# Kernel tuning notes

Measured on AMD Instinct MI355X. Metric: run time of the kernel, lower is better.

The kernel has to match this reference:

```python
import jax, jax.numpy as jnp
import numpy as np
from jax import lax

B, C, H, W = 8, 256, 64, 64
O, K, E = 256, 3, 3  # out_channels, kernel_size, num_experts

def setup_inputs() -> dict:
    key = jax.random.key(0)
    k1, k2, k3, k4, k5 = jax.random.split(key, 5)
    q = jax.random.normal(k1, (B, C, H, W), dtype=jnp.float32)
    y = jax.random.normal(k2, (B, C, H, W), dtype=jnp.float32)
    experts = jax.random.normal(k3, (E, O, 2 * C, K, K), dtype=jnp.float32)
    # torch nn.Linear(2C, E): store transposed [2C, E] for ctx @ gate_w
    bound = 1.0 / np.sqrt(2 * C)
    gate_w = jax.random.uniform(k4, (2 * C, E), minval=-bound, maxval=bound, dtype=jnp.float32)
    gate_b = jax.random.uniform(k5, (E,), minval=-bound, maxval=bound, dtype=jnp.float32)
    return {"q": q, "y": y, "experts": experts, "gate_w": gate_w, "gate_b": gate_b}

def reference(q, y, experts, gate_w, gate_b):
    # gate: softmax over experts from global-avg-pooled context of y (duplicated)
    y_ctx = jnp.mean(y, axis=(2, 3))                       # [B, C]
    context = jnp.concatenate([y_ctx, y_ctx], axis=1)       # [B, 2C]
    gates = jax.nn.softmax(context @ gate_w + gate_b, axis=1)  # [B, E]
    # per-sample fused kernel: sum_e gates[b,e] * experts[e]  -> [B, O, 2C, K, K]
    w = jnp.einsum('be,eoikl->boikl', gates, experts)
    xy = jnp.concatenate([q, q], axis=1)                     # [B, 2C, H, W]
    # batched dynamic conv via grouped conv: batch -> groups (no Python loop)
    b, c2, h, wd = xy.shape
    x1 = xy.reshape(1, b * c2, h, wd)
    w1 = w.reshape(b * O, c2, K, K)
    out = lax.conv_general_dilated(
        x1, w1, window_strides=(1, 1), padding='SAME',
        dimension_numbers=('NCHW', 'OIHW', 'NCHW'),
        feature_group_count=b)
    return out.reshape(b, O, h, wd)
```

## Files before the change

kernel.cpp:

```cpp
#include <hip/hip_runtime.h>
#include <hip/hip_bf16.h>
#include <math.h>


typedef __bf16 bf16x8 __attribute__((ext_vector_type(8)));
typedef __bf16 bf16x4 __attribute__((ext_vector_type(4)));
typedef float f32x4 __attribute__((ext_vector_type(4)));

#define AS1 __attribute__((address_space(1)))
#define AS3 __attribute__((address_space(3)))

__global__ __launch_bounds__(64) void yctx_kernel(const float* __restrict__ y,
                                                  float* __restrict__ yctx) {
  int bc = blockIdx.x;
  const float4* p = (const float4*)(y + (size_t)bc * 4096);
  int lane = threadIdx.x;
  float s = 0.f;
  for (int i = lane; i < 1024; i += 64) {
    float4 v = p[i];
    s += v.x + v.y + v.z + v.w;
  }
#pragma unroll
  for (int off = 32; off > 0; off >>= 1) s += __shfl_down(s, off, 64);
  if (lane == 0) yctx[bc] = s * (1.f / 4096.f);
}

__global__ __launch_bounds__(64) void logits_kernel(const float* __restrict__ yctx,
                                                    const float* __restrict__ gw,
                                                    const float* __restrict__ gb,
                                                    float* __restrict__ logits) {
  int be = blockIdx.x;
  int b = be / 3, e = be - b * 3;
  int lane = threadIdx.x;
  float s = 0.f;
  for (int c = lane; c < 256; c += 64)
    s += yctx[b * 256 + c] * (gw[c * 3 + e] + gw[(c + 256) * 3 + e]);
#pragma unroll
  for (int off = 32; off > 0; off >>= 1) s += __shfl_down(s, off, 64);
  if (lane == 0) logits[be] = s + gb[e];
}

__global__ __launch_bounds__(256) void wbuild_kernel(const float* __restrict__ experts,
                                                     const float* __restrict__ logits,
                                                     __bf16* __restrict__ wf) {
  int o = blockIdx.x;
  int tid = threadIdx.x;
  __shared__ float sf[3][2304];
  __shared__ float g[8][3];

#pragma unroll
  for (int e = 0; e < 3; e++) {
    const float4* src = (const float4*)(experts + ((size_t)e * 256 + o) * 4608);
    float4* dstp = (float4*)sf[e];
    for (int i = tid; i < 576; i += 256) {
      float4 a = src[i], bq = src[i + 576];
      float4 r;
      r.x = a.x + bq.x; r.y = a.y + bq.y; r.z = a.z + bq.z; r.w = a.w + bq.w;
      dstp[i] = r;
    }
  }
  if (tid < 8) {
    float l0 = logits[tid * 3 + 0], l1 = logits[tid * 3 + 1], l2 = logits[tid * 3 + 2];
    float m = fmaxf(l0, fmaxf(l1, l2));
    float e0 = __expf(l0 - m), e1 = __expf(l1 - m), e2 = __expf(l2 - m);
    float inv = 1.f / (e0 + e1 + e2);
    g[tid][0] = e0 * inv; g[tid][1] = e1 * inv; g[tid][2] = e2 * inv;
  }
  __syncthreads();

  int cl = tid & 31, ch = tid >> 5;
#pragma unroll 1
  for (int b = 0; b < 8; b++) {
    float g0 = g[b][0], g1 = g[b][1], g2 = g[b][2];
#pragma unroll
    for (int tap = 0; tap < 9; tap++) {
      float v = g0 * sf[0][tid * 9 + tap] + g1 * sf[1][tid * 9 + tap] +
                g2 * sf[2][tid * 9 + tap];
      wf[((((size_t)b * 9 + tap) * 8 + ch) * 256 + o) * 32 + cl] = (__bf16)v;
    }
  }
}

__global__ __launch_bounds__(256) void qt_kernel(const float* __restrict__ q,
                                                 __bf16* __restrict__ qT) {
  int bid = blockIdx.x;
  int hp = bid % 66;
  int t2 = bid / 66;
  int ch = t2 & 7;
  int b = t2 >> 3;
  __bf16* dst = qT + (((size_t)(b * 8 + ch) * 66 + hp) * 66) * 32;
  int tid = threadIdx.x;
  float4 z4 = {0.f, 0.f, 0.f, 0.f};
  if (hp == 0 || hp == 65) {
    float4* d4 = (float4*)dst;
    for (int i = tid; i < 264; i += 256) d4[i] = z4;
    return;
  }
  __shared__ float tile2[64][33];
  int h = hp - 1;
  {
    int w = tid & 63, ci = tid >> 6;
#pragma unroll
    for (int j = 0; j < 8; j++) {
      int c = ci * 8 + j;
      tile2[w][c] = q[(((size_t)b * 256 + ch * 32 + c) * 64 + h) * 64 + w];
    }
  }
  if (tid < 4) ((float4*)dst)[tid] = z4;
  else if (tid < 8) ((float4*)(dst + 65 * 32))[tid - 4] = z4;
  __syncthreads();

  int a = tid & 7, wsl = tid >> 3;
  int cl4 = a * 4;
#pragma unroll
  for (int k = 0; k < 2; k++) {
    int w = wsl * 2 + k, wp = w + 1;
    int clp4 = (((cl4 >> 3) ^ ((wp >> 1) & 3)) << 3) | (cl4 & 7);
    float v0 = tile2[w][cl4 + 0], v1 = tile2[w][cl4 + 1];
    float v2 = tile2[w][cl4 + 2], v3 = tile2[w][cl4 + 3];
    bf16x4 r = {(__bf16)v0, (__bf16)v1, (__bf16)v2, (__bf16)v3};
    *(bf16x4*)(dst + wp * 32 + clp4) = r;
  }
}

__global__ __launch_bounds__(256, 2) void conv_kernel(const __bf16* __restrict__ qT,
                                                      const __bf16* __restrict__ wf,
                                                      float* __restrict__ out) {
  __shared__ __align__(16) __bf16 Qlds[2][4 * 66 * 32];
  const int tid = threadIdx.x;
  const int lane = tid & 63;
  const int wv = tid >> 6;
  const int wm = wv >> 1, wn = wv & 1;
  const int l15 = lane & 15, qd = lane >> 4;

  const int bid = blockIdx.x;
  const int b = bid & 7;
  const int rem = bid >> 3;
  const int o0 = (rem >> 5) * 128;
  const int h0 = (rem & 31) * 2;

  f32x4 acc[4][4];
  {
    f32x4 z = {0.f, 0.f, 0.f, 0.f};
#pragma unroll
    for (int i = 0; i < 4; i++)
#pragma unroll
      for (int j = 0; j < 4; j++) acc[i][j] = z;
  }

  int btab[3][4];
#pragma unroll
  for (int dw = 0; dw < 3; dw++)
#pragma unroll
    for (int ni = 0; ni < 4; ni++) {
      int wp = ni * 16 + l15 + dw;
      int g = (qd ^ ((wp >> 1) & 3)) << 3;
      btab[dw][ni] = (wp * 32 + g) * 2;
    }

  const char* qT_b = (const char*)qT + (size_t)b * 8 * 66 * 66 * 32 * 2;
  const char* abase = (const char*)wf + ((size_t)b * 9 * 8 * 256 +
                                         (size_t)(o0 + wm * 64 + l15)) * 64 +
                      (size_t)qd * 16;
  bf16x8 areg[3][4];
  bf16x8 breg[2][4];

  {
    const char* qsrc = qT_b + ((size_t)h0) * 4224;
    for (int i = tid; i < 1056; i += 256) {
      int ub = i - lane;
      __builtin_amdgcn_global_load_lds((const AS1 void*)(qsrc + ((size_t)i << 4)),
                                       (AS3 void*)((char*)Qlds[0] + ((size_t)ub << 4)),
                                       16, 0, 0);
    }
#pragma unroll
    for (int mi = 0; mi < 4; mi++) {
      areg[0][mi] = *(const bf16x8*)(abase + ((size_t)(0 * 8 + 0) << 14) + mi * 1024);
      areg[1][mi] = *(const bf16x8*)(abase + ((size_t)(1 * 8 + 0) << 14) + mi * 1024);
    }
    __syncthreads();
#pragma unroll
    for (int ni = 0; ni < 4; ni++)
      breg[0][ni] = *(const bf16x8*)((const char*)Qlds[0] + wn * 4224 + btab[0][ni]);
  }

#pragma unroll 1
  for (int ch = 0; ch < 8; ch++) {
    if (ch < 7) {
      const char* qsrc = qT_b + ((size_t)((ch + 1) * 66 + h0)) * 4224;
      char* qdst = (char*)Qlds[(ch + 1) & 1];
      for (int i = tid; i < 1056; i += 256) {
        int ub = i - lane;
        __builtin_amdgcn_global_load_lds((const AS1 void*)(qsrc + ((size_t)i << 4)),
                                         (AS3 void*)(qdst + ((size_t)ub << 4)),
                                         16, 0, 0);
      }
    }
    const char* Qb = (const char*)Qlds[ch & 1];
#pragma unroll
    for (int tap = 0; tap < 9; tap++) {
      const int s = ch * 9 + tap;
      {
        int s2 = s + 2;
        int ch2 = s2 / 9, tap2 = s2 - ch2 * 9;
        if (ch2 > 7) { ch2 = 0; tap2 = 0; }
        size_t aoff = ((size_t)(tap2 * 8 + ch2)) << 14;
#pragma unroll
        for (int mi = 0; mi < 4; mi++)
          areg[(s + 2) % 3][mi] = *(const bf16x8*)(abase + aoff + mi * 1024);
      }
      if (tap < 8) {
        int tapn = tap + 1;
        int dhn = tapn / 3, dwn = tapn - dhn * 3;
        int rbn = (wn + dhn) * 4224;
#pragma unroll
        for (int ni = 0; ni < 4; ni++)
          breg[(tap + 1) & 1][ni] = *(const bf16x8*)(Qb + rbn + btab[dwn][ni]);
      }
#pragma unroll
      for (int ni = 0; ni < 4; ni++)
#pragma unroll
        for (int mi = 0; mi < 4; mi++)
          acc[mi][ni] = __builtin_amdgcn_mfma_f32_16x16x32_bf16(
              areg[s % 3][mi], breg[tap & 1][ni], acc[mi][ni], 0, 0, 0);
    }
    __syncthreads();
    if (ch < 7) {
      const char* Qn = (const char*)Qlds[(ch + 1) & 1];
#pragma unroll
      for (int ni = 0; ni < 4; ni++)
        breg[0][ni] = *(const bf16x8*)(Qn + wn * 4224 + btab[0][ni]);
    }
  }

  const int hh = h0 + wn;
#pragma unroll
  for (int mi = 0; mi < 4; mi++) {
    int o = o0 + wm * 64 + mi * 16 + qd * 4;
#pragma unroll
    for (int ni = 0; ni < 4; ni++) {
      int w = ni * 16 + l15;
#pragma unroll
      for (int rr = 0; rr < 4; rr++)
        out[(((size_t)b * 256 + (o + rr)) * 64 + hh) * 64 + w] = acc[mi][ni][rr];
    }
  }
}

extern "C" void kernel_launch(void* const* d_in, const int* in_sizes, int n_in,
                              void* d_out, int out_size, void* d_ws, size_t ws_size,
                              hipStream_t stream) {
  (void)in_sizes; (void)n_in; (void)out_size; (void)ws_size;
  const float* q = (const float*)d_in[0];
  const float* y = (const float*)d_in[1];
  const float* experts = (const float*)d_in[2];
  const float* gate_w = (const float*)d_in[3];
  const float* gate_b = (const float*)d_in[4];
  float* out = (float*)d_out;

  char* ws = (char*)d_ws;
  float* yctx = (float*)ws;
  float* logits = (float*)(ws + 8192);
  __bf16* wf = (__bf16*)(ws + 16384);
  __bf16* qT = (__bf16*)(ws + 16384 + 9437184);

  yctx_kernel<<<2048, 64, 0, stream>>>(y, yctx);
  logits_kernel<<<24, 64, 0, stream>>>(yctx, gate_w, gate_b, logits);
  qt_kernel<<<8 * 8 * 66, 256, 0, stream>>>(q, qT);
  wbuild_kernel<<<256, 256, 0, stream>>>(experts, logits, wf);
  conv_kernel<<<512, 256, 0, stream>>>(qT, wf, out);
}
```

Baseline: 182.9 us.

## Fuse prep kernels and switch conv to 32x32x16 MFMA tiles

Merges the y-mean and q-transpose kernels into one launch, and folds the gate logits computation into the weight-build kernel, cutting five launches to three. The conv kernel switches from 16x16x32 to 32x32x16 bf16 MFMA with 2x2 tiles per wave and remaps the A and B fragment offsets to match. Fewer, larger MFMAs aim to cut LDS and register fragment traffic per FLOP. The output write pattern changes to the 32x32 accumulator layout, which may coalesce differently.

```diff
diff --git a/kernel.cpp b/kernel.cpp
--- a/kernel.cpp
+++ b/kernel.cpp
@@ -6,46 +6,78 @@
 typedef __bf16 bf16x8 __attribute__((ext_vector_type(8)));
 typedef __bf16 bf16x4 __attribute__((ext_vector_type(4)));
 typedef float f32x4 __attribute__((ext_vector_type(4)));
+typedef float f32x16 __attribute__((ext_vector_type(16)));
 
 #define AS1 __attribute__((address_space(1)))
 #define AS3 __attribute__((address_space(3)))
 
-__global__ __launch_bounds__(64) void yctx_kernel(const float* __restrict__ y,
-                                                  float* __restrict__ yctx) {
-  int bc = blockIdx.x;
-  const float4* p = (const float4*)(y + (size_t)bc * 4096);
-  int lane = threadIdx.x;
-  float s = 0.f;
-  for (int i = lane; i < 1024; i += 64) {
-    float4 v = p[i];
-    s += v.x + v.y + v.z + v.w;
-  }
-#pragma unroll
-  for (int off = 32; off > 0; off >>= 1) s += __shfl_down(s, off, 64);
-  if (lane == 0) yctx[bc] = s * (1.f / 4096.f);
+__global__ __launch_bounds__(256) void prep_kernel(const float* __restrict__ q,
+                                                   const float* __restrict__ y,
+                                                   __bf16* __restrict__ qT,
+                                                   float* __restrict__ yctx) {
+  int bid = blockIdx.x;
+  int tid = threadIdx.x;
+  if (bid >= 4224) {
+    int wv = tid >> 6, lane = tid & 63;
+    int bc = (bid - 4224) * 4 + wv;
+    const float4* p = (const float4*)(y + (size_t)bc * 4096);
+    float s = 0.f;
+    for (int i = lane; i < 1024; i += 64) {
+      float4 v = p[i];
+      s += v.x + v.y + v.z + v.w;
+    }
+#pragma unroll
+    for (int off = 32; off > 0; off >>= 1) s += __shfl_down(s, off, 64);
+    if (lane == 0) yctx[bc] = s * (1.f / 4096.f);
+    return;
+  }
+  int hp = bid % 66;
+  int t2 = bid / 66;
+  int ch = t2 & 7;
+  int b = t2 >> 3;
+  __bf16* dst = qT + (((size_t)(b * 8 + ch) * 66 + hp) * 66) * 32;
+  float4 z4 = {0.f, 0.f, 0.f, 0.f};
+  if (hp == 0 || hp == 65) {
+    float4* d4 = (float4*)dst;
+    for (int i = tid; i < 264; i += 256) d4[i] = z4;
+    return;
+  }
+  __shared__ float tile2[64][33];
+  int h = hp - 1;
+  {
+    int w = tid & 63, ci = tid >> 6;
+#pragma unroll
+    for (int j = 0; j < 8; j++) {
+      int c = ci * 8 + j;
+      tile2[w][c] = q[(((size_t)b * 256 + ch * 32 + c) * 64 + h) * 64 + w];
+    }
+  }
+  if (tid < 4) ((float4*)dst)[tid] = z4;
+  else if (tid < 8) ((float4*)(dst + 65 * 32))[tid - 4] = z4;
+  __syncthreads();
+
+  int a = tid & 7, wsl = tid >> 3;
+  int cl4 = a * 4;
+#pragma unroll
+  for (int k = 0; k < 2; k++) {
+    int w = wsl * 2 + k, wp = w + 1;
+    int clp4 = (((cl4 >> 3) ^ ((wp >> 1) & 3)) << 3) | (cl4 & 7);
+    float v0 = tile2[w][cl4 + 0], v1 = tile2[w][cl4 + 1];
+    float v2 = tile2[w][cl4 + 2], v3 = tile2[w][cl4 + 3];
+    bf16x4 r = {(__bf16)v0, (__bf16)v1, (__bf16)v2, (__bf16)v3};
+    *(bf16x4*)(dst + wp * 32 + clp4) = r;
+  }
 }
 
-__global__ __launch_bounds__(64) void logits_kernel(const float* __restrict__ yctx,
-                                                    const float* __restrict__ gw,
-                                                    const float* __restrict__ gb,
-                                                    float* __restrict__ logits) {
-  int be = blockIdx.x;
-  int b = be / 3, e = be - b * 3;
-  int lane = threadIdx.x;
-  float s = 0.f;
-  for (int c = lane; c < 256; c += 64)
-    s += yctx[b * 256 + c] * (gw[c * 3 + e] + gw[(c + 256) * 3 + e]);
-#pragma unroll
-  for (int off = 32; off > 0; off >>= 1) s += __shfl_down(s, off, 64);
-  if (lane == 0) logits[be] = s + gb[e];
-}
-
 __global__ __launch_bounds__(256) void wbuild_kernel(const float* __restrict__ experts,
-                                                     const float* __restrict__ logits,
+                                                     const float* __restrict__ yctx,
+                                                     const float* __restrict__ gw,
+                                                     const float* __restrict__ gb,
                                                      __bf16* __restrict__ wf) {
   int o = blockIdx.x;
   int tid = threadIdx.x;
   __shared__ float sf[3][2304];
+  __shared__ float lgpart[4][24];
   __shared__ float g[8][3];
 
 #pragma unroll
@@ -59,8 +91,34 @@
       dstp[i] = r;
     }
   }
+  {
+    int c = tid;
+    float gwf[3], yc[8];
+#pragma unroll
+    for (int e = 0; e < 3; e++) gwf[e] = gw[c * 3 + e] + gw[(c + 256) * 3 + e];
+#pragma unroll
+    for (int b = 0; b < 8; b++) yc[b] = yctx[b * 256 + c];
+    int wv = tid >> 6, lane = tid & 63;
+#pragma unroll
+    for (int b = 0; b < 8; b++)
+#pragma unroll
+      for (int e = 0; e < 3; e++) {
+        float s = yc[b] * gwf[e];
+#pragma unroll
+        for (int off = 32; off > 0; off >>= 1) s += __shfl_down(s, off, 64);
+        if (lane == 0) lgpart[wv][b * 3 + e] = s;
+      }
+  }
+  __syncthreads();
+  if (tid < 24) {
+    int e = tid % 3;
+    float s = lgpart[0][tid] + lgpart[1][tid] + lgpart[2][tid] + lgpart[3][tid] + gb[e];
+    lgpart[0][tid] = s;
+  }
+  __syncthreads();
   if (tid < 8) {
-    float l0 = logits[tid * 3 + 0], l1 = logits[tid * 3 + 1], l2 = logits[tid * 3 + 2];
+    float l0 = lgpart[0][tid * 3 + 0], l1 = lgpart[0][tid * 3 + 1],
+          l2 = lgpart[0][tid * 3 + 2];
     float m = fmaxf(l0, fmaxf(l1, l2));
     float e0 = __expf(l0 - m), e1 = __expf(l1 - m), e2 = __expf(l2 - m);
     float inv = 1.f / (e0 + e1 + e2);
@@ -78,48 +136,6 @@
                 g2 * sf[2][tid * 9 + tap];
       wf[((((size_t)b * 9 + tap) * 8 + ch) * 256 + o) * 32 + cl] = (__bf16)v;
     }
-  }
-}
-
-__global__ __launch_bounds__(256) void qt_kernel(const float* __restrict__ q,
-                                                 __bf16* __restrict__ qT) {
-  int bid = blockIdx.x;
-  int hp = bid % 66;
-  int t2 = bid / 66;
-  int ch = t2 & 7;
-  int b = t2 >> 3;
-  __bf16* dst = qT + (((size_t)(b * 8 + ch) * 66 + hp) * 66) * 32;
-  int tid = threadIdx.x;
-  float4 z4 = {0.f, 0.f, 0.f, 0.f};
-  if (hp == 0 || hp == 65) {
-    float4* d4 = (float4*)dst;
-    for (int i = tid; i < 264; i += 256) d4[i] = z4;
-    return;
-  }
-  __shared__ float tile2[64][33];
-  int h = hp - 1;
-  {
-    int w = tid & 63, ci = tid >> 6;
-#pragma unroll
-    for (int j = 0; j < 8; j++) {
-      int c = ci * 8 + j;
-      tile2[w][c] = q[(((size_t)b * 256 + ch * 32 + c) * 64 + h) * 64 + w];
-    }
-  }
-  if (tid < 4) ((float4*)dst)[tid] = z4;
-  else if (tid < 8) ((float4*)(dst + 65 * 32))[tid - 4] = z4;
-  __syncthreads();
-
-  int a = tid & 7, wsl = tid >> 3;
-  int cl4 = a * 4;
-#pragma unroll
-  for (int k = 0; k < 2; k++) {
-    int w = wsl * 2 + k, wp = w + 1;
-    int clp4 = (((cl4 >> 3) ^ ((wp >> 1) & 3)) << 3) | (cl4 & 7);
-    float v0 = tile2[w][cl4 + 0], v1 = tile2[w][cl4 + 1];
-    float v2 = tile2[w][cl4 + 2], v3 = tile2[w][cl4 + 3];
-    bf16x4 r = {(__bf16)v0, (__bf16)v1, (__bf16)v2, (__bf16)v3};
-    *(bf16x4*)(dst + wp * 32 + clp4) = r;
   }
 }
 
@@ -131,7 +147,7 @@
   const int lane = tid & 63;
   const int wv = tid >> 6;
   const int wm = wv >> 1, wn = wv & 1;
-  const int l15 = lane & 15, qd = lane >> 4;
+  const int l31 = lane & 31, hi = lane >> 5;
 
   const int bid = blockIdx.x;
   const int b = bid & 7;
@@ -139,29 +155,31 @@
   const int o0 = (rem >> 5) * 128;
   const int h0 = (rem & 31) * 2;
 
-  f32x4 acc[4][4];
+  f32x16 acc[2][2];
   {
-    f32x4 z = {0.f, 0.f, 0.f, 0.f};
-#pragma unroll
-    for (int i = 0; i < 4; i++)
-#pragma unroll
-      for (int j = 0; j < 4; j++) acc[i][j] = z;
-  }
-
-  int btab[3][4];
+    f32x16 z = {0.f};
+#pragma unroll
+    for (int i = 0; i < 2; i++)
+#pragma unroll
+      for (int j = 0; j < 2; j++) acc[i][j] = z;
+  }
+
+  int bofs[3][2][2];
 #pragma unroll
   for (int dw = 0; dw < 3; dw++)
 #pragma unroll
-    for (int ni = 0; ni < 4; ni++) {
-      int wp = ni * 16 + l15 + dw;
-      int g = (qd ^ ((wp >> 1) & 3)) << 3;
-      btab[dw][ni] = (wp * 32 + g) * 2;
+    for (int nt = 0; nt < 2; nt++) {
+      int wp = nt * 32 + l31 + dw;
+      int sw = (wp >> 1) & 3;
+#pragma unroll
+      for (int kh = 0; kh < 2; kh++)
+        bofs[dw][nt][kh] = wp * 64 + (((kh * 2 + hi) ^ sw) << 4);
     }
 
   const char* qT_b = (const char*)qT + (size_t)b * 8 * 66 * 66 * 32 * 2;
   const char* abase = (const char*)wf + ((size_t)b * 9 * 8 * 256 +
-                                         (size_t)(o0 + wm * 64 + l15)) * 64 +
-                      (size_t)qd * 16;
+                                         (size_t)(o0 + wm * 64 + l31)) * 64 +
+                      (size_t)hi * 16;
   bf16x8 areg[3][4];
   bf16x8 breg[2][4];
 
@@ -174,14 +192,20 @@
                                        16, 0, 0);
     }
 #pragma unroll
-    for (int mi = 0; mi < 4; mi++) {
-      areg[0][mi] = *(const bf16x8*)(abase + ((size_t)(0 * 8 + 0) << 14) + mi * 1024);
-      areg[1][mi] = *(const bf16x8*)(abase + ((size_t)(1 * 8 + 0) << 14) + mi * 1024);
-    }
+    for (int mt = 0; mt < 2; mt++)
+#pragma unroll
+      for (int kh = 0; kh < 2; kh++) {
+        areg[0][mt * 2 + kh] = *(const bf16x8*)(abase + mt * 2048 + kh * 32);
+        areg[1][mt * 2 + kh] =
+            *(const bf16x8*)(abase + ((size_t)8 << 14) + mt * 2048 + kh * 32);
+      }
     __syncthreads();
 #pragma unroll
-    for (int ni = 0; ni < 4; ni++)
-      breg[0][ni] = *(const bf16x8*)((const char*)Qlds[0] + wn * 4224 + btab[0][ni]);
+    for (int kh = 0; kh < 2; kh++)
+#pragma unroll
+      for (int nt = 0; nt < 2; nt++)
+        breg[0][kh * 2 + nt] =
+            *(const bf16x8*)((const char*)Qlds[0] + wn * 4224 + bofs[0][nt][kh]);
   }
 
 #pragma unroll 1
@@ -206,43 +230,57 @@
         if (ch2 > 7) { ch2 = 0; tap2 = 0; }
         size_t aoff = ((size_t)(tap2 * 8 + ch2)) << 14;
 #pragma unroll
-        for (int mi = 0; mi < 4; mi++)
-          areg[(s + 2) % 3][mi] = *(const bf16x8*)(abase + aoff + mi * 1024);
+        for (int mt = 0; mt < 2; mt++)
+#pragma unroll
+          for (int kh = 0; kh < 2; kh++)
+            areg[(s + 2) % 3][mt * 2 + kh] =
+                *(const bf16x8*)(abase + aoff + mt * 2048 + kh * 32);
       }
       if (tap < 8) {
         int tapn = tap + 1;
         int dhn = tapn / 3, dwn = tapn - dhn * 3;
         int rbn = (wn + dhn) * 4224;
 #pragma unroll
-        for (int ni = 0; ni < 4; ni++)
-          breg[(tap + 1) & 1][ni] = *(const bf16x8*)(Qb + rbn + btab[dwn][ni]);
-      }
-#pragma unroll
-      for (int ni = 0; ni < 4; ni++)
-#pragma unroll
-        for (int mi = 0; mi < 4; mi++)
-          acc[mi][ni] = __builtin_amdgcn_mfma_f32_16x16x32_bf16(
-              areg[s % 3][mi], breg[tap & 1][ni], acc[mi][ni], 0, 0, 0);
+        for (int kh = 0; kh < 2; kh++)
+#pragma unroll
+          for (int nt = 0; nt < 2; nt++)
+            breg[(tap + 1) & 1][kh * 2 + nt] =
+                *(const bf16x8*)(Qb + rbn + bofs[dwn][nt][kh]);
+      }
+#pragma unroll
+      for (int kh = 0; kh < 2; kh++)
+#pragma unroll
+        for (int nt = 0; nt < 2; nt++)
+#pragma unroll
+          for (int mt = 0; mt < 2; mt++)
+            acc[mt][nt] = __builtin_amdgcn_mfma_f32_32x32x16_bf16(
+                areg[s % 3][mt * 2 + kh], breg[tap & 1][kh * 2 + nt],
+                acc[mt][nt], 0, 0, 0);
     }
     __syncthreads();
     if (ch < 7) {
       const char* Qn = (const char*)Qlds[(ch + 1) & 1];
 #pragma unroll
-      for (int ni = 0; ni < 4; ni++)
-        breg[0][ni] = *(const bf16x8*)(Qn + wn * 4224 + btab[0][ni]);
+      for (int kh = 0; kh < 2; kh++)
+#pragma unroll
+        for (int nt = 0; nt < 2; nt++)
+          breg[0][kh * 2 + nt] =
+              *(const bf16x8*)(Qn + wn * 4224 + bofs[0][nt][kh]);
     }
   }
 
   const int hh = h0 + wn;
 #pragma unroll
-  for (int mi = 0; mi < 4; mi++) {
-    int o = o0 + wm * 64 + mi * 16 + qd * 4;
-#pragma unroll
-    for (int ni = 0; ni < 4; ni++) {
-      int w = ni * 16 + l15;
-#pragma unroll
-      for (int rr = 0; rr < 4; rr++)
-        out[(((size_t)b * 256 + (o + rr)) * 64 + hh) * 64 + w] = acc[mi][ni][rr];
+  for (int mt = 0; mt < 2; mt++) {
+    int ob = o0 + wm * 64 + mt * 32 + 4 * hi;
+#pragma unroll
+    for (int nt = 0; nt < 2; nt++) {
+      int w = nt * 32 + l31;
+#pragma unroll
+      for (int r = 0; r < 16; r++) {
+        int o = ob + (r & 3) + 8 * (r >> 2);
+        out[(((size_t)b * 256 + o) * 64 + hh) * 64 + w] = acc[mt][nt][r];
+      }
     }
   }
 }
@@ -260,13 +298,10 @@
 
   char* ws = (char*)d_ws;
   float* yctx = (float*)ws;
-  float* logits = (float*)(ws + 8192);
   __bf16* wf = (__bf16*)(ws + 16384);
   __bf16* qT = (__bf16*)(ws + 16384 + 9437184);
 
-  yctx_kernel<<<2048, 64, 0, stream>>>(y, yctx);
-  logits_kernel<<<24, 64, 0, stream>>>(yctx, gate_w, gate_b, logits);
-  qt_kernel<<<8 * 8 * 66, 256, 0, stream>>>(q, qT);
-  wbuild_kernel<<<256, 256, 0, stream>>>(experts, logits, wf);
+  prep_kernel<<<4224 + 512, 256, 0, stream>>>(q, y, qT, yctx);
+  wbuild_kernel<<<256, 256, 0, stream>>>(experts, yctx, gate_w, gate_b, wf);
   conv_kernel<<<512, 256, 0, stream>>>(qT, wf, out);
 }
```

After: 181.6 us. About the same (-0.7%).
